# Optimization experiments

Hardware: AMD Instinct MI355X
Metric: run time of the kernel (lower is better)

Reference implementation:

```python
import jax, jax.numpy as jnp
import numpy as np
from jax import lax

B, S, N, FD = 4, 12, 307, 3
E = 64; F = 64; H = 64; K = 3; HEADS = 4; P = 12; DFF = 64


def setup_inputs() -> dict:
    key = jax.random.key(0)
    ks = jax.random.split(key, 24)
    rn = lambda i, shape, s=0.1: jax.random.normal(ks[i], shape, dtype=jnp.float32) * s
    z = lambda n: jnp.zeros((n,), jnp.float32)
    return {
        'x': jax.random.normal(ks[0], (B, S, N, FD), dtype=jnp.float32),
        'cheb': rn(1, (K, N, N), 0.05),
        'theta': rn(2, (K, E, F)),
        'W_emb_x': rn(3, (1, E)), 'b_emb_x': z(E),
        'W_emb_os': rn(4, (FD - 1, E)), 'b_emb_os': z(E),
        'U_x': rn(5, (F, 4 * H)), 'V_x': rn(6, (H, 4 * H)), 'b_x': z(4 * H),
        'U_g': rn(7, (F, 2 * H)), 'V_g': rn(8, (H, 2 * H)), 'b_g': z(2 * H),
        'W_ff1': rn(9, (H, DFF)), 'b_ff1': z(DFF), 'W_ff2': rn(10, (DFF, H)), 'b_ff2': z(H),
        'W_tc': rn(11, (F, H, 1, 3)), 'b_tc': z(F),
        'W_rc': rn(12, (F, H, 1, 1)), 'b_rc': z(F),
        'W_in': rn(13, (3 * F, F)), 'b_in': z(3 * F),
        'W_out': rn(14, (F, F)), 'b_out': z(F),
        'W_fa1': rn(15, (F, DFF)), 'b_fa1': z(DFF), 'W_fa2': rn(16, (DFF, F)), 'b_fa2': z(F),
        'W_fin': rn(17, (P, S, 1, F)), 'b_fin': z(P),
    }


def _forward(x, cheb, theta, W_emb_x, b_emb_x, W_emb_os, b_emb_os,
             U_x, V_x, b_x, U_g, V_g, b_g, W_ff1, b_ff1, W_ff2, b_ff2,
             W_tc, b_tc, W_rc, b_rc, W_in, b_in, W_out, b_out,
             W_fa1, b_fa1, W_fa2, b_fa2, W_fin, b_fin):
    # token embeddings (dropout=0 -> identity)
    emb_x = x[..., :1] @ W_emb_x + b_emb_x          # (B,S,N,E)
    emb_os = x[..., 1:] @ W_emb_os + b_emb_os       # (B,S,N,E)

    def cheb_conv(h):
        # sum_k relu-after-sum of T_k @ h @ theta_k
        agg = jnp.einsum('kmn,bsnc->kbsmc', cheb, h)
        return jax.nn.relu(jnp.einsum('kbsmc,kcd->bsmd', agg, theta))

    gcn_x = cheb_conv(emb_x)                        # (B,S,N,F)
    gcn_os = cheb_conv(emb_os)                      # (B,S,N,F)

    # Glstm: precompute input projections, scan the recurrence over time
    gx = jnp.einsum('bsnc,cf->sbnf', gcn_x, U_x) + b_x    # (S,B,N,4H)
    gg = jnp.einsum('bsnc,cf->sbnf', gcn_os, U_g) + b_g   # (S,B,N,2H)

    h0 = jnp.zeros((B, N, H), x.dtype)
    c0 = jnp.zeros((B, N, H), x.dtype)

    def step(carry, inp):
        ht, ct = carry
        gx_t, gg_t = inp
        gates = jax.nn.sigmoid(gx_t + ht @ V_x)     # ft,it,ot,ut all sigmoid (as in source)
        gov = jax.nn.sigmoid(gg_t + ht @ V_g)
        ft, it, ot, ut = jnp.split(gates, 4, axis=-1)
        gf, gu = jnp.split(gov, 2, axis=-1)
        ct = gf * ft * ct + gu * it * ut
        ht = ot * jnp.tanh(ct)
        return (ht, ct), ht

    _, hs = lax.scan(step, (h0, c0), (gx, gg))
    hidden = jnp.moveaxis(hs, 0, 1)                 # (B,S,N,H)
    # Muti_glstm output feedforward
    hidden = jax.nn.relu(hidden @ W_ff1 + b_ff1) @ W_ff2 + b_ff2

    # time conv: (1,3) kernel over time axis, pad 1
    hs_nchw = jnp.transpose(hidden, (0, 3, 2, 1))   # (B,H,N,S)
    tc = lax.conv_general_dilated(hs_nchw, W_tc, (1, 1), ((0, 0), (1, 1)),
                                  dimension_numbers=('NCHW', 'OIHW', 'NCHW'))
    tc = jnp.transpose(tc + b_tc[None, :, None, None], (0, 3, 2, 1))  # (B,S,N,F)

    # query = last time step, repeated over S
    query = jnp.broadcast_to(tc[:, -1:], (B, S, N, F))
    q_in = jnp.reshape(jnp.swapaxes(query, 2, 3), (B * N, S, F))
    kv_in = jnp.reshape(jnp.swapaxes(emb_x, 2, 3), (B * N, S, E))

    # torch MHA (batch_first=False): seq axis is dim0 (L=B*N), batch axis is dim1 (S)
    hd = F // HEADS
    Wq, Wk, Wv = jnp.split(W_in, 3, axis=0)
    bq, bk, bv = jnp.split(b_in, 3)

    def proj(t, Wp, bp):
        L = t.shape[0]
        p = t @ Wp.T + bp                            # (L, S, F)
        return jnp.transpose(p.reshape(L, S * HEADS, hd), (1, 0, 2))  # (S*HEADS, L, hd)

    qh = proj(q_in, Wq, bq)
    kh = proj(kv_in, Wk, bk)
    vh = proj(kv_in, Wv, bv)
    scores = jnp.einsum('hld,hmd->hlm', qh, kh) / np.float32(np.sqrt(hd))
    attn = jax.nn.softmax(scores, axis=-1)
    ctx = jnp.einsum('hlm,hmd->hld', attn, vh)       # (S*HEADS, B*N, hd)
    ctx = jnp.transpose(ctx, (1, 0, 2)).reshape(B * N, S, F)
    dsa = ctx @ W_out.T + b_out                      # (B*N, S, F)

    dsa = jnp.swapaxes(dsa.reshape(B, N, S, F), 1, 2)  # (B,S,N,F)
    ffa = jax.nn.relu(dsa @ W_fa1 + b_fa1) @ W_fa2 + b_fa2
    # residual 1x1 conv over channels of hidden
    res = jnp.einsum('bsnh,fh->bsnf', hidden, W_rc[:, :, 0, 0]) + b_rc
    comb = res + ffa                                 # (B,S,N,F)
    # final conv: channels=S, kernel (1,F) valid, then take last width index
    out = jnp.einsum('bsnf,psf->bpn', comb, W_fin[:, :, 0, :]) + b_fin[None, :, None]
    return out                                       # (B, pre_len, N)


def reference(x, cheb, theta, W_emb_x, b_emb_x, W_emb_os, b_emb_os,
              U_x, V_x, b_x, U_g, V_g, b_g, W_ff1, b_ff1, W_ff2, b_ff2,
              W_tc, b_tc, W_rc, b_rc, W_in, b_in, W_out, b_out,
              W_fa1, b_fa1, W_fa2, b_fa2, W_fin, b_fin):
    return _forward(x, cheb, theta, W_emb_x, b_emb_x, W_emb_os, b_emb_os,
                    U_x, V_x, b_x, U_g, V_g, b_g, W_ff1, b_ff1, W_ff2, b_ff2,
                    W_tc, b_tc, W_rc, b_rc, W_in, b_in, W_out, b_out,
                    W_fa1, b_fa1, W_fa2, b_fa2, W_fin, b_fin)
```

## Files before the change

kernel.cpp:

```cpp
#include <hip/hip_runtime.h>
#include <hip/hip_bf16.h>

#define BB 4
#define SS 12
#define NN 307
#define LL 1228
#define BSC 48
#define GG 48
#define WS_CX    0
#define WS_CROW  132624
#define WS_TXD   133568
#define WS_TBD   133760
#define WS_T1D   133952
#define WS_T2D   134144
#define WS_TOB   134336
#define WS_WRCT  134528
#define WS_WOT   138624
#define WS_H2    142720
#define WS_TFL   1085824
#define WS_XFL   1164416
#define WS_QH    2107520
#define WS_KH    3050624
#define WS_VH    3993728
#define WS_CTX   4936832

__global__ __launch_bounds__(320) void k12_fused(
    const float* __restrict__ x, const float* __restrict__ cheb,
    const float* __restrict__ theta, const float* __restrict__ Wex,
    const float* __restrict__ bex, const float* __restrict__ Weos,
    const float* __restrict__ beos, const float* __restrict__ W_rc,
    const float* __restrict__ W_out, float* __restrict__ ws) {
  int blk = blockIdx.x;
  int tid = threadIdx.x;
  if (blk < 144) {
    int k = blk / BSC, bs = blk % BSC;
    __shared__ float xl[921];
    for (int i = tid; i < 921; i += 320) xl[i] = x[bs * 921 + i];
    __syncthreads();
    int m = tid;
    if (m < NN) {
      const float* ch = cheb + (k * NN + m) * NN;
      float a0 = 0.f, a1 = 0.f, a2 = 0.f, ar = 0.f;
      for (int n = 0; n < NN; ++n) {
        float c = ch[n];
        ar += c;
        a0 = fmaf(c, xl[3 * n], a0);
        a1 = fmaf(c, xl[3 * n + 1], a1);
        a2 = fmaf(c, xl[3 * n + 2], a2);
      }
      ws[WS_CX + ((k * 3 + 0) * BSC + bs) * NN + m] = a0;
      ws[WS_CX + ((k * 3 + 1) * BSC + bs) * NN + m] = a1;
      ws[WS_CX + ((k * 3 + 2) * BSC + bs) * NN + m] = a2;
      if (bs == 0) ws[WS_CROW + k * NN + m] = ar;
    }
  } else if (blk < 3092) {
    int idx = (blk - 144) * 320 + tid;
    if (idx < 943104) {
      int n = idx % NN;
      int t = idx / NN;
      int e = t & 63;
      int bs = t >> 6;
      ws[WS_XFL + idx] = fmaf(x[(bs * NN + n) * 3], Wex[e], bex[e]);
    }
  } else {
    if (tid < 192) {
      int k = tid / 64, d = tid % 64;
      float a0 = 0.f, a1 = 0.f, a2 = 0.f, a3 = 0.f, a4 = 0.f;
      for (int c = 0; c < 64; ++c) {
        float th = theta[(k * 64 + c) * 64 + d];
        a0 = fmaf(Wex[c], th, a0);
        a1 = fmaf(bex[c], th, a1);
        a2 = fmaf(Weos[c], th, a2);
        a3 = fmaf(Weos[64 + c], th, a3);
        a4 = fmaf(beos[c], th, a4);
      }
      ws[WS_TXD + tid] = a0; ws[WS_TBD + tid] = a1; ws[WS_T1D + tid] = a2;
      ws[WS_T2D + tid] = a3; ws[WS_TOB + tid] = a4;
    }
    for (int i = tid; i < 4096; i += 320) {
      int hh = i >> 6, f = i & 63;
      ws[WS_WRCT + i] = W_rc[f * 64 + hh];
      ws[WS_WOT + i]  = W_out[f * 64 + hh];
    }
  }
}

__global__ __launch_bounds__(384) void k3_scan(
    const float* __restrict__ U_x, const float* __restrict__ V_x,
    const float* __restrict__ b_x, const float* __restrict__ U_g,
    const float* __restrict__ V_g, const float* __restrict__ b_g,
    const float* __restrict__ W_ff1, const float* __restrict__ b_ff1,
    const float* __restrict__ W_ff2, const float* __restrict__ b_ff2,
    const float* __restrict__ W_tc, const float* __restrict__ b_tc,
    float* __restrict__ ws) {
  int l = blockIdx.x;
  int b = l / NN, n = l % NN;
  int tid = threadIdx.x;
  __shared__ float gcx[768], gcos[768], hsb[768], sg[256], sv[128];

  for (int idx = tid; idx < 768; idx += 384) {
    int s = idx >> 6, d = idx & 63;
    int bs = b * SS + s;
    float ax = 0.f, ao = 0.f;
#pragma unroll
    for (int k = 0; k < 3; ++k) {
      float c0 = ws[WS_CX + ((k * 3 + 0) * BSC + bs) * NN + n];
      float c1 = ws[WS_CX + ((k * 3 + 1) * BSC + bs) * NN + n];
      float c2 = ws[WS_CX + ((k * 3 + 2) * BSC + bs) * NN + n];
      float cr = ws[WS_CROW + k * NN + n];
      ax += c0 * ws[WS_TXD + k * 64 + d] + cr * ws[WS_TBD + k * 64 + d];
      ao += c1 * ws[WS_T1D + k * 64 + d] + c2 * ws[WS_T2D + k * 64 + d] +
            cr * ws[WS_TOB + k * 64 + d];
    }
    gcx[idx] = fmaxf(ax, 0.f);
    gcos[idx] = fmaxf(ao, 0.f);
  }
  __syncthreads();

  float gr[12];
  float vcol[64];
  if (tid < 256) {
#pragma unroll
    for (int s = 0; s < 12; ++s) gr[s] = b_x[tid];
    for (int c4 = 0; c4 < 16; ++c4) {
      float u0 = U_x[(4 * c4 + 0) * 256 + tid];
      float u1 = U_x[(4 * c4 + 1) * 256 + tid];
      float u2 = U_x[(4 * c4 + 2) * 256 + tid];
      float u3 = U_x[(4 * c4 + 3) * 256 + tid];
#pragma unroll
      for (int s = 0; s < 12; ++s) {
        float4 g = *reinterpret_cast<const float4*>(&gcx[s * 64 + 4 * c4]);
        gr[s] = fmaf(g.x, u0, fmaf(g.y, u1, fmaf(g.z, u2, fmaf(g.w, u3, gr[s]))));
      }
    }
#pragma unroll
    for (int c = 0; c < 64; ++c) vcol[c] = V_x[c * 256 + tid];
  } else {
    int j2 = tid - 256;
#pragma unroll
    for (int s = 0; s < 12; ++s) gr[s] = b_g[j2];
    for (int c4 = 0; c4 < 16; ++c4) {
      float u0 = U_g[(4 * c4 + 0) * 128 + j2];
      float u1 = U_g[(4 * c4 + 1) * 128 + j2];
      float u2 = U_g[(4 * c4 + 2) * 128 + j2];
      float u3 = U_g[(4 * c4 + 3) * 128 + j2];
#pragma unroll
      for (int s = 0; s < 12; ++s) {
        float4 g = *reinterpret_cast<const float4*>(&gcos[s * 64 + 4 * c4]);
        gr[s] = fmaf(g.x, u0, fmaf(g.y, u1, fmaf(g.z, u2, fmaf(g.w, u3, gr[s]))));
      }
    }
#pragma unroll
    for (int c = 0; c < 64; ++c) vcol[c] = V_g[c * 128 + j2];
  }

  float ct = 0.f;
  for (int s = 0; s < 12; ++s) {
    float a = gr[s];
    if (s > 0) {
      const float* hp = &hsb[(s - 1) * 64];
      float a0 = 0.f, a1 = 0.f, a2 = 0.f, a3 = 0.f;
#pragma unroll
      for (int c4 = 0; c4 < 16; c4 += 4) {
        float4 h0 = *reinterpret_cast<const float4*>(&hp[4 * c4]);
        float4 h1 = *reinterpret_cast<const float4*>(&hp[4 * c4 + 4]);
        float4 h2 = *reinterpret_cast<const float4*>(&hp[4 * c4 + 8]);
        float4 h3 = *reinterpret_cast<const float4*>(&hp[4 * c4 + 12]);
        a0 = fmaf(h0.x, vcol[4 * c4 + 0], fmaf(h0.y, vcol[4 * c4 + 1],
             fmaf(h0.z, vcol[4 * c4 + 2], fmaf(h0.w, vcol[4 * c4 + 3], a0))));
        a1 = fmaf(h1.x, vcol[4 * c4 + 4], fmaf(h1.y, vcol[4 * c4 + 5],
             fmaf(h1.z, vcol[4 * c4 + 6], fmaf(h1.w, vcol[4 * c4 + 7], a1))));
        a2 = fmaf(h2.x, vcol[4 * c4 + 8], fmaf(h2.y, vcol[4 * c4 + 9],
             fmaf(h2.z, vcol[4 * c4 + 10], fmaf(h2.w, vcol[4 * c4 + 11], a2))));
        a3 = fmaf(h3.x, vcol[4 * c4 + 12], fmaf(h3.y, vcol[4 * c4 + 13],
             fmaf(h3.z, vcol[4 * c4 + 14], fmaf(h3.w, vcol[4 * c4 + 15], a3))));
      }
      a += (a0 + a1) + (a2 + a3);
    }
    float sig = 1.f / (1.f + __expf(-a));
    if (tid < 256) sg[tid] = sig; else sv[tid - 256] = sig;
    __syncthreads();
    if (tid < 64) {
      ct = sv[tid] * sg[tid] * ct + sv[64 + tid] * sg[64 + tid] * sg[192 + tid];
      hsb[s * 64 + tid] = sg[128 + tid] * tanhf(ct);
    }
    __syncthreads();
  }

  for (int idx = tid; idx < 768; idx += 384) {
    int s = idx >> 6, d = idx & 63;
    float acc = b_ff1[d];
    for (int c4 = 0; c4 < 16; ++c4) {
      float4 h4 = *reinterpret_cast<const float4*>(&hsb[s * 64 + 4 * c4]);
      acc = fmaf(h4.x, W_ff1[(4 * c4 + 0) * 64 + d],
            fmaf(h4.y, W_ff1[(4 * c4 + 1) * 64 + d],
            fmaf(h4.z, W_ff1[(4 * c4 + 2) * 64 + d],
            fmaf(h4.w, W_ff1[(4 * c4 + 3) * 64 + d], acc))));
    }
    gcx[idx] = fmaxf(acc, 0.f);
  }
  __syncthreads();
  for (int idx = tid; idx < 768; idx += 384) {
    int s = idx >> 6, h = idx & 63;
    float acc = b_ff2[h];
    for (int c4 = 0; c4 < 16; ++c4) {
      float4 t4 = *reinterpret_cast<const float4*>(&gcx[s * 64 + 4 * c4]);
      acc = fmaf(t4.x, W_ff2[(4 * c4 + 0) * 64 + h],
            fmaf(t4.y, W_ff2[(4 * c4 + 1) * 64 + h],
            fmaf(t4.z, W_ff2[(4 * c4 + 2) * 64 + h],
            fmaf(t4.w, W_ff2[(4 * c4 + 3) * 64 + h], acc))));
    }
    ws[WS_H2 + ((b * SS + s) * NN + n) * 64 + h] = acc;
    gcos[idx] = acc;
  }
  __syncthreads();
  if (tid < 64) {
    int f = tid;
    float acc = b_tc[f];
    for (int h = 0; h < 64; ++h) {
      acc = fmaf(gcos[10 * 64 + h], W_tc[(f * 64 + h) * 3 + 0], acc);
      acc = fmaf(gcos[11 * 64 + h], W_tc[(f * 64 + h) * 3 + 1], acc);
    }
    ws[WS_TFL + (b * 64 + f) * NN + n] = acc;
  }
}

__global__ __launch_bounds__(256) void k5_qkv(const float* __restrict__ W_in,
                                              const float* __restrict__ b_in,
                                              float* __restrict__ ws) {
  int blk = blockIdx.x;
  int g = blk / 77, mt = blk % 77;
  int s = g >> 2, a = g & 3;
  int m0 = mt * 16;
  __shared__ float xw[16][64], qw[16][64];
  for (int i = threadIdx.x; i < 1024; i += 256) {
    int mi = i >> 6, e = i & 63;
    int m = m0 + mi;
    if (m < LL) {
      int base = m * 768 + s * 64;
      xw[mi][e] = ws[WS_XFL + base + e];
      int bq = base / 235776;
      int off = base % 19648;
      qw[mi][e] = ws[WS_TFL + bq * 19648 + off + e];
    }
  }
  __syncthreads();
  int mi = threadIdx.x >> 4, d = threadIdx.x & 15;
  int m = m0 + mi;
  if (m < LL) {
    int f = a * 16 + d;
    float aq = b_in[f], ak = b_in[64 + f], av = b_in[128 + f];
    for (int e = 0; e < 64; ++e) {
      aq = fmaf(qw[mi][e], W_in[f * 64 + e], aq);
      ak = fmaf(xw[mi][e], W_in[(64 + f) * 64 + e], ak);
      av = fmaf(xw[mi][e], W_in[(128 + f) * 64 + e], av);
    }
    int o = (g * LL + m) * 16 + d;
    ws[WS_QH + o] = aq; ws[WS_KH + o] = ak; ws[WS_VH + o] = av;
  }
}

__global__ __launch_bounds__(512) void k6_attn(float* __restrict__ ws) {
  int blk = blockIdx.x;
  int g = blk / 10, qt = blk % 10;
  int s = g >> 2, a = g & 3;
  int tid = threadIdx.x;
  int w = tid >> 6;
  int qi = tid & 63;
  int l0 = qt * 128 + qi;
  int l1 = l0 + 64;
  bool act0 = (l0 < LL), act1 = (l1 < LL);

  __shared__ float sh[9728];
  float4* kt4 = reinterpret_cast<float4*>(sh);
  float4* vt4 = reinterpret_cast<float4*>(sh + 4096);

  float q0[16], q1[16], cx0[16], cx1[16];
  if (act0) {
    const float4* qp = reinterpret_cast<const float4*>(ws + WS_QH + (g * LL + l0) * 16);
#pragma unroll
    for (int jj = 0; jj < 4; ++jj) {
      float4 t = qp[jj];
      q0[4 * jj] = t.x * 0.25f; q0[4 * jj + 1] = t.y * 0.25f;
      q0[4 * jj + 2] = t.z * 0.25f; q0[4 * jj + 3] = t.w * 0.25f;
    }
  } else {
#pragma unroll
    for (int d = 0; d < 16; ++d) q0[d] = 0.f;
  }
  if (act1) {
    const float4* qp = reinterpret_cast<const float4*>(ws + WS_QH + (g * LL + l1) * 16);
#pragma unroll
    for (int jj = 0; jj < 4; ++jj) {
      float4 t = qp[jj];
      q1[4 * jj] = t.x * 0.25f; q1[4 * jj + 1] = t.y * 0.25f;
      q1[4 * jj + 2] = t.z * 0.25f; q1[4 * jj + 3] = t.w * 0.25f;
    }
  } else {
#pragma unroll
    for (int d = 0; d < 16; ++d) q1[d] = 0.f;
  }
#pragma unroll
  for (int d = 0; d < 16; ++d) { cx0[d] = 0.f; cx1[d] = 0.f; }
  float den0 = 0.f, den1 = 0.f;

  const float4* kb = reinterpret_cast<const float4*>(ws + WS_KH + g * LL * 16);
  const float4* vb = reinterpret_cast<const float4*>(ws + WS_VH + g * LL * 16);

  for (int mt = 0; mt < 5; ++mt) {
    int mbase = mt * 256;
    int cnt = LL - mbase; if (cnt > 256) cnt = 256;
    int nf4 = cnt * 4;
    for (int i = tid; i < nf4; i += 512) {
      kt4[i] = kb[mbase * 4 + i];
      vt4[i] = vb[mbase * 4 + i];
    }
    __syncthreads();
    int e0 = w * 32;
    int e1 = e0 + 32; if (e1 > cnt) e1 = cnt;
    for (int mi = e0; mi < e1; ++mi) {
      float4 ka = kt4[mi * 4], kbb = kt4[mi * 4 + 1];
      float4 kc = kt4[mi * 4 + 2], kd = kt4[mi * 4 + 3];
      float p0 = q0[0] * ka.x, p1 = q1[0] * ka.x;
      p0 = fmaf(q0[1], ka.y, p0);   p1 = fmaf(q1[1], ka.y, p1);
      p0 = fmaf(q0[2], ka.z, p0);   p1 = fmaf(q1[2], ka.z, p1);
      p0 = fmaf(q0[3], ka.w, p0);   p1 = fmaf(q1[3], ka.w, p1);
      p0 = fmaf(q0[4], kbb.x, p0);  p1 = fmaf(q1[4], kbb.x, p1);
      p0 = fmaf(q0[5], kbb.y, p0);  p1 = fmaf(q1[5], kbb.y, p1);
      p0 = fmaf(q0[6], kbb.z, p0);  p1 = fmaf(q1[6], kbb.z, p1);
      p0 = fmaf(q0[7], kbb.w, p0);  p1 = fmaf(q1[7], kbb.w, p1);
      p0 = fmaf(q0[8], kc.x, p0);   p1 = fmaf(q1[8], kc.x, p1);
      p0 = fmaf(q0[9], kc.y, p0);   p1 = fmaf(q1[9], kc.y, p1);
      p0 = fmaf(q0[10], kc.z, p0);  p1 = fmaf(q1[10], kc.z, p1);
      p0 = fmaf(q0[11], kc.w, p0);  p1 = fmaf(q1[11], kc.w, p1);
      p0 = fmaf(q0[12], kd.x, p0);  p1 = fmaf(q1[12], kd.x, p1);
      p0 = fmaf(q0[13], kd.y, p0);  p1 = fmaf(q1[13], kd.y, p1);
      p0 = fmaf(q0[14], kd.z, p0);  p1 = fmaf(q1[14], kd.z, p1);
      p0 = fmaf(q0[15], kd.w, p0);  p1 = fmaf(q1[15], kd.w, p1);
      float e0w = __expf(fminf(p0, 60.f));
      float e1w = __expf(fminf(p1, 60.f));
      den0 += e0w; den1 += e1w;
      float4 va = vt4[mi * 4], vbb = vt4[mi * 4 + 1];
      float4 vc = vt4[mi * 4 + 2], vd = vt4[mi * 4 + 3];
      cx0[0]  = fmaf(e0w, va.x, cx0[0]);   cx1[0]  = fmaf(e1w, va.x, cx1[0]);
      cx0[1]  = fmaf(e0w, va.y, cx0[1]);   cx1[1]  = fmaf(e1w, va.y, cx1[1]);
      cx0[2]  = fmaf(e0w, va.z, cx0[2]);   cx1[2]  = fmaf(e1w, va.z, cx1[2]);
      cx0[3]  = fmaf(e0w, va.w, cx0[3]);   cx1[3]  = fmaf(e1w, va.w, cx1[3]);
      cx0[4]  = fmaf(e0w, vbb.x, cx0[4]);  cx1[4]  = fmaf(e1w, vbb.x, cx1[4]);
      cx0[5]  = fmaf(e0w, vbb.y, cx0[5]);  cx1[5]  = fmaf(e1w, vbb.y, cx1[5]);
      cx0[6]  = fmaf(e0w, vbb.z, cx0[6]);  cx1[6]  = fmaf(e1w, vbb.z, cx1[6]);
      cx0[7]  = fmaf(e0w, vbb.w, cx0[7]);  cx1[7]  = fmaf(e1w, vbb.w, cx1[7]);
      cx0[8]  = fmaf(e0w, vc.x, cx0[8]);   cx1[8]  = fmaf(e1w, vc.x, cx1[8]);
      cx0[9]  = fmaf(e0w, vc.y, cx0[9]);   cx1[9]  = fmaf(e1w, vc.y, cx1[9]);
      cx0[10] = fmaf(e0w, vc.z, cx0[10]);  cx1[10] = fmaf(e1w, vc.z, cx1[10]);
      cx0[11] = fmaf(e0w, vc.w, cx0[11]);  cx1[11] = fmaf(e1w, vc.w, cx1[11]);
      cx0[12] = fmaf(e0w, vd.x, cx0[12]);  cx1[12] = fmaf(e1w, vd.x, cx1[12]);
      cx0[13] = fmaf(e0w, vd.y, cx0[13]);  cx1[13] = fmaf(e1w, vd.y, cx1[13]);
      cx0[14] = fmaf(e0w, vd.z, cx0[14]);  cx1[14] = fmaf(e1w, vd.z, cx1[14]);
      cx0[15] = fmaf(e0w, vd.w, cx0[15]);  cx1[15] = fmaf(e1w, vd.w, cx1[15]);
    }
    __syncthreads();
  }

  float* sden = sh;
  float* scx  = sh + 512;
#pragma unroll
  for (int ph = 0; ph < 2; ++ph) {
    sden[w * 64 + qi] = ph ? den1 : den0;
    const float* cxp = ph ? cx1 : cx0;
#pragma unroll
    for (int d = 0; d < 16; ++d) scx[(w * 64 + qi) * 17 + d] = cxp[d];
    __syncthreads();
    if (tid < 256) {
      int q2 = tid >> 2, jj = tid & 3;
      int l2 = qt * 128 + ph * 64 + q2;
      if (l2 < LL) {
        float dtot = 0.f, c0 = 0.f, c1 = 0.f, c2 = 0.f, c3 = 0.f;
#pragma unroll
        for (int u = 0; u < 8; ++u) {
          dtot += sden[u * 64 + q2];
          const float* cp = &scx[(u * 64 + q2) * 17 + jj * 4];
          c0 += cp[0]; c1 += cp[1]; c2 += cp[2]; c3 += cp[3];
        }
        float inv = 1.f / dtot;
        float* op = ws + WS_CTX + (l2 * SS + s) * 64 + a * 16 + jj * 4;
        *reinterpret_cast<float4*>(op) =
            make_float4(c0 * inv, c1 * inv, c2 * inv, c3 * inv);
      }
    }
    __syncthreads();
  }
}

__global__ __launch_bounds__(64) void k7a_comb(
    const float* __restrict__ W_fa1, const float* __restrict__ b_fa1,
    const float* __restrict__ W_fa2, const float* __restrict__ b_fa2,
    const float* __restrict__ b_rc, const float* __restrict__ b_out,
    float* __restrict__ ws) {
  int blk = blockIdx.x;
  int l = blk / SS, s = blk % SS;
  int b = l / NN, n = l % NN;
  int f = threadIdx.x;
  __shared__ float h2r[64], ctr[64], dsrL[64], trL[64];

  h2r[f] = ws[WS_H2 + ((b * SS + s) * NN + n) * 64 + f];
  ctr[f] = ws[WS_CTX + (l * SS + s) * 64 + f];
  __syncthreads();

  float dsr = b_out[f], res = b_rc[f];
  for (int q = 0; q < 64; ++q) {
    dsr = fmaf(ctr[q], ws[WS_WOT + q * 64 + f], dsr);
    res = fmaf(h2r[q], ws[WS_WRCT + q * 64 + f], res);
  }
  dsrL[f] = dsr;
  __syncthreads();

  float t = b_fa1[f];
  for (int q = 0; q < 64; ++q) t = fmaf(dsrL[q], W_fa1[q * 64 + f], t);
  trL[f] = fmaxf(t, 0.f);
  __syncthreads();

  float ff = b_fa2[f];
  for (int q = 0; q < 64; ++q) ff = fmaf(trL[q], W_fa2[q * 64 + f], ff);
  ws[WS_XFL + (l * SS + s) * 64 + f] = res + ff;
}

__global__ __launch_bounds__(320) void k7b_fin(
    const float* __restrict__ W_fin, const float* __restrict__ b_fin,
    const float* __restrict__ ws, float* __restrict__ out) {
  int blk = blockIdx.x;
  int b = blk / SS, p = blk % SS;
  int tid = threadIdx.x;
  __shared__ float wf[768];
  for (int i = tid; i < 768; i += 320) wf[i] = W_fin[p * 768 + i];
  __syncthreads();
  int n = tid;
  if (n < NN) {
    const float* cb = ws + WS_XFL + (b * NN + n) * 768;
    float a0 = 0.f, a1 = 0.f, a2 = 0.f, a3 = 0.f;
    for (int i = 0; i < 768; i += 4) {
      a0 = fmaf(cb[i], wf[i], a0);
      a1 = fmaf(cb[i + 1], wf[i + 1], a1);
      a2 = fmaf(cb[i + 2], wf[i + 2], a2);
      a3 = fmaf(cb[i + 3], wf[i + 3], a3);
    }
    out[(b * SS + p) * NN + n] = (a0 + a1) + (a2 + a3) + b_fin[p];
  }
}

extern "C" void kernel_launch(void* const* d_in, const int* in_sizes, int n_in,
                              void* d_out, int out_size, void* d_ws, size_t ws_size,
                              hipStream_t stream) {
  (void)in_sizes; (void)n_in; (void)out_size; (void)ws_size;
  const float* x     = (const float*)d_in[0];
  const float* cheb  = (const float*)d_in[1];
  const float* theta = (const float*)d_in[2];
  const float* Wex   = (const float*)d_in[3];
  const float* bex   = (const float*)d_in[4];
  const float* Weos  = (const float*)d_in[5];
  const float* beos  = (const float*)d_in[6];
  const float* U_x   = (const float*)d_in[7];
  const float* V_x   = (const float*)d_in[8];
  const float* b_x   = (const float*)d_in[9];
  const float* U_g   = (const float*)d_in[10];
  const float* V_g   = (const float*)d_in[11];
  const float* b_g   = (const float*)d_in[12];
  const float* W_ff1 = (const float*)d_in[13];
  const float* b_ff1 = (const float*)d_in[14];
  const float* W_ff2 = (const float*)d_in[15];
  const float* b_ff2 = (const float*)d_in[16];
  const float* W_tc  = (const float*)d_in[17];
  const float* b_tc  = (const float*)d_in[18];
  const float* W_rc  = (const float*)d_in[19];
  const float* b_rc  = (const float*)d_in[20];
  const float* W_in  = (const float*)d_in[21];
  const float* b_in  = (const float*)d_in[22];
  const float* W_out = (const float*)d_in[23];
  const float* b_out = (const float*)d_in[24];
  const float* W_fa1 = (const float*)d_in[25];
  const float* b_fa1 = (const float*)d_in[26];
  const float* W_fa2 = (const float*)d_in[27];
  const float* b_fa2 = (const float*)d_in[28];
  const float* W_fin = (const float*)d_in[29];
  const float* b_fin = (const float*)d_in[30];
  float* ws = (float*)d_ws;
  float* outp = (float*)d_out;

  k12_fused<<<3093, 320, 0, stream>>>(x, cheb, theta, Wex, bex, Weos, beos,
                                      W_rc, W_out, ws);
  k3_scan<<<1228, 384, 0, stream>>>(U_x, V_x, b_x, U_g, V_g, b_g,
                                    W_ff1, b_ff1, W_ff2, b_ff2, W_tc, b_tc, ws);
  k5_qkv<<<48 * 77, 256, 0, stream>>>(W_in, b_in, ws);
  k6_attn<<<480, 512, 0, stream>>>(ws);
  k7a_comb<<<LL * SS, 64, 0, stream>>>(W_fa1, b_fa1, W_fa2, b_fa2,
                                       b_rc, b_out, ws);
  k7b_fin<<<BB * SS, 320, 0, stream>>>(W_fin, b_fin, ws, outp);
}
```

Measured before the change: 352.7 us.

## Fold K/V projections into the scan kernel as extra blocks

Moves the K and V input projections, which depend only on the embedding output, into the LSTM scan launch as additional blocks so they can run concurrently with the latency-bound recurrence. The Q projection, which needs the scan's temporal-conv output, stays in a separate smaller kernel. This trades some idle threads in the extra blocks and a unified shared buffer for better device occupancy during the scan.

```diff
diff --git a/kernel.cpp b/kernel.cpp
--- a/kernel.cpp
+++ b/kernel.cpp
@@ -85,18 +85,56 @@
   }
 }
 
-__global__ __launch_bounds__(384) void k3_scan(
+__global__ __launch_bounds__(384) void kB_scan_kv(
     const float* __restrict__ U_x, const float* __restrict__ V_x,
     const float* __restrict__ b_x, const float* __restrict__ U_g,
     const float* __restrict__ V_g, const float* __restrict__ b_g,
     const float* __restrict__ W_ff1, const float* __restrict__ b_ff1,
     const float* __restrict__ W_ff2, const float* __restrict__ b_ff2,
     const float* __restrict__ W_tc, const float* __restrict__ b_tc,
+    const float* __restrict__ W_in, const float* __restrict__ b_in,
     float* __restrict__ ws) {
-  int l = blockIdx.x;
+  __shared__ float sh[2688];
+  int blk = blockIdx.x;
+  int tid = threadIdx.x;
+
+  if (blk >= 1228) {
+    int bb = blk - 1228;
+    int g = bb / 77, mt = bb % 77;
+    int s = g >> 2, a = g & 3;
+    int m0 = mt * 16;
+    float* xw = sh;
+    for (int i = tid; i < 1024; i += 384) {
+      int mi = i >> 6, e = i & 63;
+      int m = m0 + mi;
+      if (m < LL) xw[i] = ws[WS_XFL + m * 768 + s * 64 + e];
+    }
+    __syncthreads();
+    if (tid < 256) {
+      int mi = tid >> 4, d = tid & 15;
+      int m = m0 + mi;
+      if (m < LL) {
+        int f = a * 16 + d;
+        float ak = b_in[64 + f], av = b_in[128 + f];
+        const float* xr = &xw[mi * 64];
+        for (int e = 0; e < 64; ++e) {
+          ak = fmaf(xr[e], W_in[(64 + f) * 64 + e], ak);
+          av = fmaf(xr[e], W_in[(128 + f) * 64 + e], av);
+        }
+        int o = (g * LL + m) * 16 + d;
+        ws[WS_KH + o] = ak; ws[WS_VH + o] = av;
+      }
+    }
+    return;
+  }
+
+  float* gcx = sh;
+  float* gcos = sh + 768;
+  float* hsb = sh + 1536;
+  float* sg = sh + 2304;
+  float* sv = sh + 2560;
+  int l = blk;
   int b = l / NN, n = l % NN;
-  int tid = threadIdx.x;
-  __shared__ float gcx[768], gcos[768], hsb[768], sg[256], sv[128];
 
   for (int idx = tid; idx < 768; idx += 384) {
     int s = idx >> 6, d = idx & 63;
@@ -225,23 +263,22 @@
   }
 }
 
-__global__ __launch_bounds__(256) void k5_qkv(const float* __restrict__ W_in,
-                                              const float* __restrict__ b_in,
-                                              float* __restrict__ ws) {
+__global__ __launch_bounds__(256) void k5q(const float* __restrict__ W_in,
+                                           const float* __restrict__ b_in,
+                                           float* __restrict__ ws) {
   int blk = blockIdx.x;
   int g = blk / 77, mt = blk % 77;
   int s = g >> 2, a = g & 3;
   int m0 = mt * 16;
-  __shared__ float xw[16][64], qw[16][64];
+  __shared__ float qw[1024];
   for (int i = threadIdx.x; i < 1024; i += 256) {
     int mi = i >> 6, e = i & 63;
     int m = m0 + mi;
     if (m < LL) {
       int base = m * 768 + s * 64;
-      xw[mi][e] = ws[WS_XFL + base + e];
       int bq = base / 235776;
       int off = base % 19648;
-      qw[mi][e] = ws[WS_TFL + bq * 19648 + off + e];
+      qw[i] = ws[WS_TFL + bq * 19648 + off + e];
     }
   }
   __syncthreads();
@@ -249,14 +286,10 @@
   int m = m0 + mi;
   if (m < LL) {
     int f = a * 16 + d;
-    float aq = b_in[f], ak = b_in[64 + f], av = b_in[128 + f];
-    for (int e = 0; e < 64; ++e) {
-      aq = fmaf(qw[mi][e], W_in[f * 64 + e], aq);
-      ak = fmaf(xw[mi][e], W_in[(64 + f) * 64 + e], ak);
-      av = fmaf(xw[mi][e], W_in[(128 + f) * 64 + e], av);
-    }
-    int o = (g * LL + m) * 16 + d;
-    ws[WS_QH + o] = aq; ws[WS_KH + o] = ak; ws[WS_VH + o] = av;
+    float aq = b_in[f];
+    const float* qr = &qw[mi * 64];
+    for (int e = 0; e < 64; ++e) aq = fmaf(qr[e], W_in[f * 64 + e], aq);
+    ws[WS_QH + (g * LL + m) * 16 + d] = aq;
   }
 }
 
@@ -488,9 +521,10 @@
 
   k12_fused<<<3093, 320, 0, stream>>>(x, cheb, theta, Wex, bex, Weos, beos,
                                       W_rc, W_out, ws);
-  k3_scan<<<1228, 384, 0, stream>>>(U_x, V_x, b_x, U_g, V_g, b_g,
-                                    W_ff1, b_ff1, W_ff2, b_ff2, W_tc, b_tc, ws);
-  k5_qkv<<<48 * 77, 256, 0, stream>>>(W_in, b_in, ws);
+  kB_scan_kv<<<1228 + 3696, 384, 0, stream>>>(U_x, V_x, b_x, U_g, V_g, b_g,
+                                              W_ff1, b_ff1, W_ff2, b_ff2,
+                                              W_tc, b_tc, W_in, b_in, ws);
+  k5q<<<3696, 256, 0, stream>>>(W_in, b_in, ws);
   k6_attn<<<480, 512, 0, stream>>>(ws);
   k7a_comb<<<LL * SS, 64, 0, stream>>>(W_fa1, b_fa1, W_fa2, b_fa2,
                                        b_rc, b_out, ws);
```

New measurement: 367.6 us. 1.04x slower.
